# Kernel tuning notes

Hardware: AMD Instinct MI355X
Metric: run time of the kernel (lower is better)

Reference implementation:

```python
import jax, jax.numpy as jnp
import numpy as np
from jax import lax

B, W_LEN, V, E, C, K, L = 8, 1000, 50000, 100, 50, 3, 18000


def setup_inputs() -> dict:
    key = jax.random.key(0)
    ks = jax.random.split(key, 7)
    return {
        "x": jax.random.randint(ks[0], (B, W_LEN), 0, V),
        "W_embed": jax.random.normal(ks[1], (V, E), dtype=jnp.float32) * 0.1,
        "conv_w": jax.random.normal(ks[2], (C, E, K), dtype=jnp.float32) * 0.08,
        "conv_b": jax.random.normal(ks[3], (C,), dtype=jnp.float32) * 0.01,
        "u_w": jax.random.normal(ks[4], (L, C), dtype=jnp.float32) * 0.1,
        "out_w": jax.random.normal(ks[5], (L, C), dtype=jnp.float32) * 0.1,
        "out_b": jax.random.normal(ks[6], (L,), dtype=jnp.float32) * 0.01,
    }


def reference(x, W_embed, conv_w, conv_b, u_w, out_w, out_b):
    # embedding lookup: (B, W, E)
    emb = W_embed[x]
    # conv1d over sequence, 'same' padding: (B, C, W)
    emb_ncw = jnp.transpose(emb, (0, 2, 1))
    H = lax.conv_general_dilated(
        emb_ncw, conv_w, window_strides=(1,), padding=[(K // 2, K // 2)],
        dimension_numbers=("NCH", "OIH", "NCH"))
    H = jnp.tanh(H + conv_b[None, :, None])
    H = jnp.transpose(H, (0, 2, 1))  # (B, W, C)
    # label-wise attention scores: (B, L, W), softmax over seq
    scores = jnp.einsum("lc,bwc->blw", u_w, H)
    attns = jax.nn.softmax(scores, axis=2)
    # attention-pooled reps: (B, L, C)
    m = jnp.einsum("blw,bwc->blc", attns, H)
    # per-label weighted dot product + bias, sigmoid: (B, L)
    out = jax.nn.sigmoid(jnp.sum(out_w[None] * m, axis=2) + out_b[None])
    return out
```

## Files before the change

kernel.cpp:

```cpp
#include <hip/hip_runtime.h>
#include <hip/hip_bf16.h>
#include <cmath>

#define AS1 __attribute__((address_space(1)))
#define AS3 __attribute__((address_space(3)))

#define B_ 8
#define W_LEN_ 1000
#define WP 1024
#define E_ 100
#define C_ 50
#define CPAD 64
#define HP 72
#define K_ 3
#define L_ 18000
#define TL 64
#define NLBLK ((L_ + TL - 1) / TL)
#define CWT 16
#define NSLOT (K_ * (E_ / 4))

typedef __attribute__((ext_vector_type(8))) short bf16x8;
typedef __attribute__((ext_vector_type(4))) short bf16x4;
typedef __attribute__((ext_vector_type(4))) float f32x4;

static __device__ __forceinline__ float bf2f(short s) {
    return __uint_as_float(((unsigned)(unsigned short)s) << 16);
}

__global__ __launch_bounds__(256) void prep_all(
    const float* __restrict__ conv_w, const float* __restrict__ u_w,
    const float* __restrict__ out_w,
    bf16x4* __restrict__ cwTs, __hip_bfloat16* __restrict__ UO)
{
    int tid = blockIdx.x * blockDim.x + threadIdx.x;
    if (tid < NSLOT * C_) {
        int slot = tid / C_;
        int c    = tid % C_;
        int k = slot / (E_ / 4);
        int i = slot % (E_ / 4);
        bf16x4 v;
        #pragma unroll
        for (int q = 0; q < 4; q++) {
            __hip_bfloat16 h = __float2bfloat16(conv_w[((size_t)c * E_ + 4 * i + q) * K_ + k]);
            v[q] = *reinterpret_cast<short*>(&h);
        }
        cwTs[tid] = v;
    }
    if (tid < 2 * L_ * CPAD) {
        int c = tid & (CPAD - 1);
        int l = (tid >> 6) % L_;
        int m = tid / (L_ * CPAD);
        const float* src = m ? out_w : u_w;
        float v = (c < C_) ? src[(size_t)l * C_ + c] : 0.f;
        UO[tid] = __float2bfloat16(v);
    }
}

__global__ __launch_bounds__(256) void conv_kernel(
    const int* __restrict__ x,
    const float* __restrict__ W_embed,
    const bf16x4* __restrict__ cwTs,
    const float* __restrict__ conv_b,
    __hip_bfloat16* __restrict__ H)
{
    __shared__ float4 emb_s[(CWT + 2) * (E_ / 4)];
    __shared__ bf16x4 wS[NSLOT * C_];

    const int b  = blockIdx.y;
    const int w0 = blockIdx.x * CWT;
    const int tid = threadIdx.x;

    for (int i = tid; i < NSLOT * C_; i += 256) wS[i] = cwTs[i];

    for (int i = tid; i < (CWT + 2) * (E_ / 4); i += 256) {
        int row = i / (E_ / 4);
        int e4  = i % (E_ / 4);
        int ws  = w0 - 1 + row;
        float4 v = make_float4(0.f, 0.f, 0.f, 0.f);
        if ((unsigned)ws < (unsigned)W_LEN_)
            v = ((const float4*)(W_embed + (size_t)x[b * W_LEN_ + ws] * E_))[e4];
        emb_s[i] = v;
    }
    __syncthreads();

    const int c  = tid & 63;
    const int wq = tid >> 6;
    const int cc = (c < C_) ? c : 0;

    f32x4 acc[4];
    const float bias = conv_b[cc];
    #pragma unroll
    for (int j = 0; j < 4; j++) acc[j] = (f32x4){bias, 0.f, 0.f, 0.f};

    const float4* eb = &emb_s[wq * 4 * (E_ / 4)];

    #pragma unroll 5
    for (int i = 0; i < E_ / 4; i++) {
        bf16x4 kb0 = wS[i * C_ + cc];
        bf16x4 kb1 = wS[(25 + i) * C_ + cc];
        bf16x4 kb2 = wS[(50 + i) * C_ + cc];
        float4 k0 = make_float4(bf2f(kb0[0]), bf2f(kb0[1]), bf2f(kb0[2]), bf2f(kb0[3]));
        float4 k1 = make_float4(bf2f(kb1[0]), bf2f(kb1[1]), bf2f(kb1[2]), bf2f(kb1[3]));
        float4 k2 = make_float4(bf2f(kb2[0]), bf2f(kb2[1]), bf2f(kb2[2]), bf2f(kb2[3]));
        float4 e0 = eb[i],       e1 = eb[25 + i],  e2 = eb[50 + i];
        float4 e3 = eb[75 + i],  e4 = eb[100 + i], e5 = eb[125 + i];
        acc[0].x += e0.x*k0.x + e1.x*k1.x + e2.x*k2.x;
        acc[0].y += e0.y*k0.y + e1.y*k1.y + e2.y*k2.y;
        acc[0].z += e0.z*k0.z + e1.z*k1.z + e2.z*k2.z;
        acc[0].w += e0.w*k0.w + e1.w*k1.w + e2.w*k2.w;
        acc[1].x += e1.x*k0.x + e2.x*k1.x + e3.x*k2.x;
        acc[1].y += e1.y*k0.y + e2.y*k1.y + e3.y*k2.y;
        acc[1].z += e1.z*k0.z + e2.z*k1.z + e3.z*k2.z;
        acc[1].w += e1.w*k0.w + e2.w*k1.w + e3.w*k2.w;
        acc[2].x += e2.x*k0.x + e3.x*k1.x + e4.x*k2.x;
        acc[2].y += e2.y*k0.y + e3.y*k1.y + e4.y*k2.y;
        acc[2].z += e2.z*k0.z + e3.z*k1.z + e4.z*k2.z;
        acc[2].w += e2.w*k0.w + e3.w*k1.w + e4.w*k2.w;
        acc[3].x += e3.x*k0.x + e4.x*k1.x + e5.x*k2.x;
        acc[3].y += e3.y*k0.y + e4.y*k1.y + e5.y*k2.y;
        acc[3].z += e3.z*k0.z + e4.z*k1.z + e5.z*k2.z;
        acc[3].w += e3.w*k0.w + e4.w*k1.w + e5.w*k2.w;
    }

    #pragma unroll
    for (int j = 0; j < 4; j++) {
        int w = w0 + wq * 4 + j;
        float v = 0.f;
        if (c < C_ && w < W_LEN_)
            v = tanhf((acc[j].x + acc[j].z) + (acc[j].y + acc[j].w));
        __hip_bfloat16* row = H + ((size_t)b * WP + w) * HP;
        row[c] = __float2bfloat16(v);
        if (c < HP - 64) row[64 + c] = __float2bfloat16(0.f);
    }
}

__global__ __launch_bounds__(256) void attn_kernel(
    const __hip_bfloat16* __restrict__ H,
    const __hip_bfloat16* __restrict__ UO,
    const float* __restrict__ out_b,
    float* __restrict__ out)
{
    __shared__ float2 red[2][TL];

    const int b  = blockIdx.y;
    const int l0 = blockIdx.x * TL;
    const int tid  = threadIdx.x;
    const int lane = tid & 63;
    const int wid  = tid >> 6;
    const int mi = wid & 1, ni = wid >> 1;
    const int col = lane & 15, quad = lane >> 4;

    bf16x8 Uf[2][2], Of[2][2];
    #pragma unroll
    for (int mt = 0; mt < 2; mt++) {
        int l = l0 + mi * 32 + mt * 16 + col;
        if (l >= L_) l = L_ - 1;
        const __hip_bfloat16* up = UO + (size_t)l * CPAD + quad * 8;
        const __hip_bfloat16* op = up + (size_t)L_ * CPAD;
        #pragma unroll
        for (int st = 0; st < 2; st++) {
            Uf[mt][st] = *(const bf16x8*)(up + st * 32);
            Of[mt][st] = *(const bf16x8*)(op + st * 32);
        }
    }

    f32x4 lsum[2] = {{0.f,0.f,0.f,0.f},{0.f,0.f,0.f,0.f}};
    f32x4 num [2] = {{0.f,0.f,0.f,0.f},{0.f,0.f,0.f,0.f}};
    const f32x4 zero = {0.f, 0.f, 0.f, 0.f};

    const char* gB = (const char*)(H + (size_t)b * WP * HP)
                   + ((size_t)(ni * 32 + col) * HP + quad * 8) * 2;

#define WSTEP (64 * HP * 2)

#define LOADF(Bf, gp)                                                            \
    {                                                                            \
        const char* _g = (gp);                                                   \
        _Pragma("unroll")                                                        \
        for (int nt = 0; nt < 2; nt++)                                           \
            _Pragma("unroll")                                                    \
            for (int st = 0; st < 2; st++)                                       \
                Bf[nt][st] = *(const bf16x8*)(_g + nt * (16 * HP * 2) + st * 64);\
    }

#define COMPUTE(Bf)                                                              \
    _Pragma("unroll")                                                            \
    for (int nt = 0; nt < 2; nt++) {                                             \
        _Pragma("unroll")                                                        \
        for (int mt = 0; mt < 2; mt++) {                                         \
            __builtin_amdgcn_s_setprio(1);                                       \
            f32x4 S = __builtin_amdgcn_mfma_f32_16x16x32_bf16(Uf[mt][0], Bf[nt][0], zero, 0, 0, 0); \
            S       = __builtin_amdgcn_mfma_f32_16x16x32_bf16(Uf[mt][1], Bf[nt][1], S,    0, 0, 0); \
            f32x4 T = __builtin_amdgcn_mfma_f32_16x16x32_bf16(Of[mt][0], Bf[nt][0], zero, 0, 0, 0); \
            T       = __builtin_amdgcn_mfma_f32_16x16x32_bf16(Of[mt][1], Bf[nt][1], T,    0, 0, 0); \
            __builtin_amdgcn_s_setprio(0);                                       \
            _Pragma("unroll")                                                    \
            for (int r = 0; r < 4; r++) {                                        \
                float p = __builtin_amdgcn_exp2f(S[r] * 1.4426950408889634f);    \
                lsum[mt][r] += p;                                                \
                num [mt][r] += p * T[r];                                         \
            }                                                                    \
        }                                                                        \
    }

    bf16x8 Ba[2][2], Bb[2][2];
    LOADF(Ba, gB)

    #pragma unroll 1
    for (int t = 0; t < WP / 64; t += 2) {
        LOADF(Bb, gB + WSTEP)
        COMPUTE(Ba)
        if (t + 2 < WP / 64)
            LOADF(Ba, gB + 2 * WSTEP)
        COMPUTE(Bb)
        gB += 2 * WSTEP;
    }

    #pragma unroll
    for (int mt = 0; mt < 2; mt++) {
        #pragma unroll
        for (int r = 0; r < 4; r++) {
            float ls = lsum[mt][r], nm = num[mt][r];
            #pragma unroll
            for (int d = 1; d < 16; d <<= 1) {
                ls += __shfl_xor(ls, d, 64);
                nm += __shfl_xor(nm, d, 64);
            }
            if (col == 0)
                red[ni][mi * 32 + mt * 16 + quad * 4 + r] = make_float2(ls, nm);
        }
    }
    __syncthreads();

    if (tid < TL) {
        int l = l0 + tid;
        if (l < L_) {
            float2 p0 = red[0][tid], p1 = red[1][tid];
            float z = (p0.y + p1.y) / (p0.x + p1.x - (float)(WP - W_LEN_)) + out_b[l];
            out[(size_t)b * L_ + l] = 1.f / (1.f + __expf(-z));
        }
    }
}

extern "C" void kernel_launch(void* const* d_in, const int* in_sizes, int n_in,
                              void* d_out, int out_size, void* d_ws, size_t ws_size,
                              hipStream_t stream) {
    const int*   x       = (const int*)  d_in[0];
    const float* W_embed = (const float*)d_in[1];
    const float* conv_w  = (const float*)d_in[2];
    const float* conv_b  = (const float*)d_in[3];
    const float* u_w     = (const float*)d_in[4];
    const float* out_w   = (const float*)d_in[5];
    const float* out_b   = (const float*)d_in[6];
    float* out = (float*)d_out;

    char* ws = (char*)d_ws;
    __hip_bfloat16* H  = (__hip_bfloat16*)ws;
    __hip_bfloat16* UO = (__hip_bfloat16*)(ws + 1179648);
    bf16x4*       cwTs = (bf16x4*)(ws + 1179648 + 4608000);

    {
        const int total = 2 * L_ * CPAD;
        prep_all<<<dim3((total + 255) / 256), 256, 0, stream>>>(conv_w, u_w, out_w, cwTs, UO);
    }
    {
        dim3 grid(WP / CWT, B_);
        conv_kernel<<<grid, 256, 0, stream>>>(x, W_embed, cwTs, conv_b, H);
    }
    {
        dim3 grid(NLBLK, B_);
        attn_kernel<<<grid, 256, 0, stream>>>(H, UO, out_b, out);
    }
}
```

Baseline: 148.1 us.

## Give each wave all 64 labels and a 16-column W slice; shrink H row pitch to 64

The attention kernel's wave decomposition changes. Each wave now holds U/O fragments for all 64 labels in the tile and streams its own 16-row slice of H, instead of a 2x2 split over labels and sequence positions. This halves the H fragment loads per wave and reuses each loaded B fragment across four label tiles. The cost is more VGPRs for the Uf/Of/accumulator arrays and a 4-way reduction in shared memory. The H row pitch also drops from 72 to 64, which removes the padding-zero stores and shrinks the buffer, at the risk of LDS/cache bank alignment effects.

```diff
diff --git a/kernel.cpp b/kernel.cpp
--- a/kernel.cpp
+++ b/kernel.cpp
@@ -11,7 +11,7 @@
 #define E_ 100
 #define C_ 50
 #define CPAD 64
-#define HP 72
+#define HP 64
 #define K_ 3
 #define L_ 18000
 #define TL 64
@@ -130,7 +130,6 @@
             v = tanhf((acc[j].x + acc[j].z) + (acc[j].y + acc[j].w));
         __hip_bfloat16* row = H + ((size_t)b * WP + w) * HP;
         row[c] = __float2bfloat16(v);
-        if (c < HP - 64) row[64 + c] = __float2bfloat16(0.f);
     }
 }
 
@@ -140,20 +139,19 @@
     const float* __restrict__ out_b,
     float* __restrict__ out)
 {
-    __shared__ float2 red[2][TL];
+    __shared__ float2 red[4][TL];
 
     const int b  = blockIdx.y;
     const int l0 = blockIdx.x * TL;
     const int tid  = threadIdx.x;
     const int lane = tid & 63;
     const int wid  = tid >> 6;
-    const int mi = wid & 1, ni = wid >> 1;
     const int col = lane & 15, quad = lane >> 4;
 
-    bf16x8 Uf[2][2], Of[2][2];
-    #pragma unroll
-    for (int mt = 0; mt < 2; mt++) {
-        int l = l0 + mi * 32 + mt * 16 + col;
+    bf16x8 Uf[4][2], Of[4][2];
+    #pragma unroll
+    for (int mt = 0; mt < 4; mt++) {
+        int l = l0 + mt * 16 + col;
         if (l >= L_) l = L_ - 1;
         const __hip_bfloat16* up = UO + (size_t)l * CPAD + quad * 8;
         const __hip_bfloat16* op = up + (size_t)L_ * CPAD;
@@ -164,46 +162,40 @@
         }
     }
 
-    f32x4 lsum[2] = {{0.f,0.f,0.f,0.f},{0.f,0.f,0.f,0.f}};
-    f32x4 num [2] = {{0.f,0.f,0.f,0.f},{0.f,0.f,0.f,0.f}};
+    f32x4 lsum[4] = {{0.f,0.f,0.f,0.f},{0.f,0.f,0.f,0.f},{0.f,0.f,0.f,0.f},{0.f,0.f,0.f,0.f}};
+    f32x4 num [4] = {{0.f,0.f,0.f,0.f},{0.f,0.f,0.f,0.f},{0.f,0.f,0.f,0.f},{0.f,0.f,0.f,0.f}};
     const f32x4 zero = {0.f, 0.f, 0.f, 0.f};
 
     const char* gB = (const char*)(H + (size_t)b * WP * HP)
-                   + ((size_t)(ni * 32 + col) * HP + quad * 8) * 2;
+                   + ((size_t)(wid * 16 + col) * HP + quad * 8) * 2;
 
 #define WSTEP (64 * HP * 2)
 
 #define LOADF(Bf, gp)                                                            \
     {                                                                            \
         const char* _g = (gp);                                                   \
-        _Pragma("unroll")                                                        \
-        for (int nt = 0; nt < 2; nt++)                                           \
-            _Pragma("unroll")                                                    \
-            for (int st = 0; st < 2; st++)                                       \
-                Bf[nt][st] = *(const bf16x8*)(_g + nt * (16 * HP * 2) + st * 64);\
+        Bf[0] = *(const bf16x8*)(_g);                                            \
+        Bf[1] = *(const bf16x8*)(_g + 64);                                       \
     }
 
 #define COMPUTE(Bf)                                                              \
     _Pragma("unroll")                                                            \
-    for (int nt = 0; nt < 2; nt++) {                                             \
+    for (int mt = 0; mt < 4; mt++) {                                             \
+        __builtin_amdgcn_s_setprio(1);                                           \
+        f32x4 S = __builtin_amdgcn_mfma_f32_16x16x32_bf16(Uf[mt][0], Bf[0], zero, 0, 0, 0); \
+        S       = __builtin_amdgcn_mfma_f32_16x16x32_bf16(Uf[mt][1], Bf[1], S,    0, 0, 0); \
+        f32x4 T = __builtin_amdgcn_mfma_f32_16x16x32_bf16(Of[mt][0], Bf[0], zero, 0, 0, 0); \
+        T       = __builtin_amdgcn_mfma_f32_16x16x32_bf16(Of[mt][1], Bf[1], T,    0, 0, 0); \
+        __builtin_amdgcn_s_setprio(0);                                           \
         _Pragma("unroll")                                                        \
-        for (int mt = 0; mt < 2; mt++) {                                         \
-            __builtin_amdgcn_s_setprio(1);                                       \
-            f32x4 S = __builtin_amdgcn_mfma_f32_16x16x32_bf16(Uf[mt][0], Bf[nt][0], zero, 0, 0, 0); \
-            S       = __builtin_amdgcn_mfma_f32_16x16x32_bf16(Uf[mt][1], Bf[nt][1], S,    0, 0, 0); \
-            f32x4 T = __builtin_amdgcn_mfma_f32_16x16x32_bf16(Of[mt][0], Bf[nt][0], zero, 0, 0, 0); \
-            T       = __builtin_amdgcn_mfma_f32_16x16x32_bf16(Of[mt][1], Bf[nt][1], T,    0, 0, 0); \
-            __builtin_amdgcn_s_setprio(0);                                       \
-            _Pragma("unroll")                                                    \
-            for (int r = 0; r < 4; r++) {                                        \
-                float p = __builtin_amdgcn_exp2f(S[r] * 1.4426950408889634f);    \
-                lsum[mt][r] += p;                                                \
-                num [mt][r] += p * T[r];                                         \
-            }                                                                    \
+        for (int r = 0; r < 4; r++) {                                            \
+            float p = __builtin_amdgcn_exp2f(S[r] * 1.4426950408889634f);        \
+            lsum[mt][r] += p;                                                    \
+            num [mt][r] += p * T[r];                                             \
         }                                                                        \
     }
 
-    bf16x8 Ba[2][2], Bb[2][2];
+    bf16x8 Ba[2], Bb[2];
     LOADF(Ba, gB)
 
     #pragma unroll 1
@@ -217,7 +209,7 @@
     }
 
     #pragma unroll
-    for (int mt = 0; mt < 2; mt++) {
+    for (int mt = 0; mt < 4; mt++) {
         #pragma unroll
         for (int r = 0; r < 4; r++) {
             float ls = lsum[mt][r], nm = num[mt][r];
@@ -227,7 +219,7 @@
                 nm += __shfl_xor(nm, d, 64);
             }
             if (col == 0)
-                red[ni][mi * 32 + mt * 16 + quad * 4 + r] = make_float2(ls, nm);
+                red[wid][mt * 16 + quad * 4 + r] = make_float2(ls, nm);
         }
     }
     __syncthreads();
@@ -235,8 +227,9 @@
     if (tid < TL) {
         int l = l0 + tid;
         if (l < L_) {
-            float2 p0 = red[0][tid], p1 = red[1][tid];
-            float z = (p0.y + p1.y) / (p0.x + p1.x - (float)(WP - W_LEN_)) + out_b[l];
+            float ls = red[0][tid].x + red[1][tid].x + red[2][tid].x + red[3][tid].x;
+            float nm = red[0][tid].y + red[1][tid].y + red[2][tid].y + red[3][tid].y;
+            float z = nm / (ls - (float)(WP - W_LEN_)) + out_b[l];
             out[(size_t)b * L_ + l] = 1.f / (1.f + __expf(-z));
         }
     }
@@ -256,8 +249,8 @@
 
     char* ws = (char*)d_ws;
     __hip_bfloat16* H  = (__hip_bfloat16*)ws;
-    __hip_bfloat16* UO = (__hip_bfloat16*)(ws + 1179648);
-    bf16x4*       cwTs = (bf16x4*)(ws + 1179648 + 4608000);
+    __hip_bfloat16* UO = (__hip_bfloat16*)(ws + 1048576);
+    bf16x4*       cwTs = (bf16x4*)(ws + 1048576 + 4608000);
 
     {
         const int total = 2 * L_ * CPAD;
```

Result: slower. 165.7 us (+11.9%).

## Shrink H row pitch to 64 and deepen attention prefetch to four buffers

Applied to the files above, without the earlier changes.

Reduces the padded H row stride from 72 to 64 bf16, drops the writes that zeroed the extra padding, and shifts the workspace offsets to match. The attention kernel's software pipeline goes from double to quadruple register buffering, keeping three tiles in flight ahead of compute, and the exp/accumulate step is written in vector form. The aim is less H traffic and better hiding of global load latency. The cost is higher register pressure, and a power-of-two stride could cause cache or channel conflicts.

```diff
diff --git a/kernel.cpp b/kernel.cpp
--- a/kernel.cpp
+++ b/kernel.cpp
@@ -11,7 +11,7 @@
 #define E_ 100
 #define C_ 50
 #define CPAD 64
-#define HP 72
+#define HP 64
 #define K_ 3
 #define L_ 18000
 #define TL 64
@@ -130,7 +130,6 @@
             v = tanhf((acc[j].x + acc[j].z) + (acc[j].y + acc[j].w));
         __hip_bfloat16* row = H + ((size_t)b * WP + w) * HP;
         row[c] = __float2bfloat16(v);
-        if (c < HP - 64) row[64 + c] = __float2bfloat16(0.f);
     }
 }
 
@@ -172,10 +171,11 @@
                    + ((size_t)(ni * 32 + col) * HP + quad * 8) * 2;
 
 #define WSTEP (64 * HP * 2)
-
-#define LOADF(Bf, gp)                                                            \
+#define NSTEP (WP / 64)
+
+#define LOADF(Bf, step)                                                          \
     {                                                                            \
-        const char* _g = (gp);                                                   \
+        const char* _g = gB + (size_t)(step) * WSTEP;                            \
         _Pragma("unroll")                                                        \
         for (int nt = 0; nt < 2; nt++)                                           \
             _Pragma("unroll")                                                    \
@@ -194,26 +194,30 @@
             f32x4 T = __builtin_amdgcn_mfma_f32_16x16x32_bf16(Of[mt][0], Bf[nt][0], zero, 0, 0, 0); \
             T       = __builtin_amdgcn_mfma_f32_16x16x32_bf16(Of[mt][1], Bf[nt][1], T,    0, 0, 0); \
             __builtin_amdgcn_s_setprio(0);                                       \
+            f32x4 p;                                                             \
             _Pragma("unroll")                                                    \
-            for (int r = 0; r < 4; r++) {                                        \
-                float p = __builtin_amdgcn_exp2f(S[r] * 1.4426950408889634f);    \
-                lsum[mt][r] += p;                                                \
-                num [mt][r] += p * T[r];                                         \
-            }                                                                    \
+            for (int r = 0; r < 4; r++)                                          \
+                p[r] = __builtin_amdgcn_exp2f(S[r] * 1.4426950408889634f);       \
+            lsum[mt] = lsum[mt] + p;                                             \
+            num [mt] = num [mt] + p * T;                                         \
         }                                                                        \
     }
 
-    bf16x8 Ba[2][2], Bb[2][2];
-    LOADF(Ba, gB)
+    bf16x8 B0[2][2], B1[2][2], B2[2][2], B3[2][2];
+    LOADF(B0, 0)
+    LOADF(B1, 1)
+    LOADF(B2, 2)
 
     #pragma unroll 1
-    for (int t = 0; t < WP / 64; t += 2) {
-        LOADF(Bb, gB + WSTEP)
-        COMPUTE(Ba)
-        if (t + 2 < WP / 64)
-            LOADF(Ba, gB + 2 * WSTEP)
-        COMPUTE(Bb)
-        gB += 2 * WSTEP;
+    for (int t = 0; t < NSTEP; t += 4) {
+        if (t + 3 < NSTEP) LOADF(B3, t + 3)
+        COMPUTE(B0)
+        if (t + 4 < NSTEP) LOADF(B0, t + 4)
+        COMPUTE(B1)
+        if (t + 5 < NSTEP) LOADF(B1, t + 5)
+        COMPUTE(B2)
+        if (t + 6 < NSTEP) LOADF(B2, t + 6)
+        COMPUTE(B3)
     }
 
     #pragma unroll
@@ -256,8 +260,8 @@
 
     char* ws = (char*)d_ws;
     __hip_bfloat16* H  = (__hip_bfloat16*)ws;
-    __hip_bfloat16* UO = (__hip_bfloat16*)(ws + 1179648);
-    bf16x4*       cwTs = (bf16x4*)(ws + 1179648 + 4608000);
+    __hip_bfloat16* UO = (__hip_bfloat16*)(ws + 1048576);
+    bf16x4*       cwTs = (bf16x4*)(ws + 1048576 + 4608000);
 
     {
         const int total = 2 * L_ * CPAD;
```

New measurement: 196.8 us. 32.9% more time.
